# Kernel optimization log

Hardware: AMD Instinct MI355X
Metric: run time of the kernel (lower is better)

Reference implementation:

```python
import jax, jax.numpy as jnp
import numpy as np

KS = 3        # opt.kernel_size
B = 8         # batch
T = 512       # total_length (frames)
CQ = 126      # motion channels
CK = 80       # music channels
H = 128       # hid_c
SLOPE = 0.2   # lrelu slope in ConvBlock
INF = jnp.float32(1e30)


def _conv_block(x, w, b):
    # x: [B, Cin, T]; w: [Cout, Cin, KS]; reflect pad, stride 1, lrelu
    xp = jnp.pad(x, ((0, 0), (0, 0), (1, 1)), mode='reflect')
    y = jax.lax.conv_general_dilated(xp, w, (1,), 'VALID',
                                     dimension_numbers=('NCH', 'OIH', 'NCH'))
    return jax.nn.leaky_relu(y + b[None, :, None], SLOPE)


def _encode(x, params):
    for w, b in params:
        x = _conv_block(x, w, b)
    return x  # [B, H, T]


def _dtw_single(d, L):
    # d: [M, N] cost matrix, L: scalar int valid length. Returns 0/1 path matrix.
    M, N = d.shape
    jcol = jnp.arange(N)
    # row 0: cumulative along j, predecessor is 'left' (choice 1)
    row0 = jnp.cumsum(d[0])
    ch0 = jnp.where(jcol == 0, -1, 1).astype(jnp.int32)

    def row_step(prev_row, d_row):
        p_diag = jnp.concatenate([jnp.full((1,), INF), prev_row[:-1]])

        def inner(left, xs):
            pd, pu, dij, j = xs
            m = jnp.minimum(jnp.minimum(pd, left), pu)
            # tie-break order matches numpy code: diag, then left, then up
            choice = jnp.where(pd == m, 0, jnp.where(left == m, 1, 2)).astype(jnp.int32)
            cost = m + dij
            cost = jnp.where(j == 0, pu + dij, cost)      # first column: from up
            choice = jnp.where(j == 0, 2, choice)
            return cost, (cost, choice)

        _, (crow, chrow) = jax.lax.scan(inner, INF, (p_diag, prev_row, d_row, jcol))
        return crow, chrow

    _, chs = jax.lax.scan(row_step, row0, d[1:])
    choices = jnp.concatenate([ch0[None], chs], axis=0)  # [M, N]

    path01 = jnp.zeros((M, N), jnp.float32).at[L - 1, L - 1].set(1.0)

    def bt_step(carry, _):
        ix, iy, p = carry
        active = (ix > 0) | (iy > 0)
        c = choices[ix, iy]
        nix = jnp.where(c == 0, ix - 1, jnp.where(c == 1, ix, ix - 1))
        niy = jnp.where(c == 0, iy - 1, jnp.where(c == 1, iy - 1, iy))
        nix = jnp.where(active, nix, ix)
        niy = jnp.where(active, niy, iy)
        p = p.at[nix, niy].set(jnp.where(active, 1.0, p[nix, niy]))
        return (nix, niy, p), None

    (_, _, path01), _ = jax.lax.scan(bt_step, (L - 1, L - 1, path01), None,
                                     length=2 * M - 2)
    return path01


def setup_inputs() -> dict:
    key = jax.random.key(0)
    ks = jax.random.split(key, 16)

    def w(k, o, i):
        return jax.random.normal(k, (o, i, KS), jnp.float32) * np.float32(np.sqrt(2.0 / (i * KS)))

    inp = {
        'vec': jax.random.normal(ks[0], (B, CQ, T), jnp.float32),
        'music': jax.random.normal(ks[1], (B, CK, T), jnp.float32),
        'real_length': jax.random.randint(ks[2], (B,), T // 2, T + 1, jnp.int32),
        'qw1': w(ks[3], CQ, CQ), 'qb1': jnp.zeros((CQ,), jnp.float32),
        'qw2': w(ks[4], H, CQ),  'qb2': jnp.zeros((H,), jnp.float32),
        'qw3': w(ks[5], H, H),   'qb3': jnp.zeros((H,), jnp.float32),
        'kw1': w(ks[6], CK, CK), 'kb1': jnp.zeros((CK,), jnp.float32),
        'kw2': w(ks[7], H, CK),  'kb2': jnp.zeros((H,), jnp.float32),
        'kw3': w(ks[8], H, H),   'kb3': jnp.zeros((H,), jnp.float32),
    }
    return inp


def reference(vec, music, real_length, qw1, qb1, qw2, qb2, qw3, qb3,
              kw1, kb1, kw2, kb2, kw3, kb3):
    # conv encoders (ConvBlock x3 each)
    q = _encode(vec, [(qw1, qb1), (qw2, qb2), (qw3, qb3)])    # [B, H, T]
    k = _encode(music, [(kw1, kb1), (kw2, kb2), (kw3, kb3)])  # [B, H, T]
    qf = q.transpose(0, 2, 1)  # [B, N, H] motion latent
    kf = k.transpose(0, 2, 1)  # [B, M, H] music latent
    # Euclidean_dist(music_feat=kf, motion_feat=qf): dist[b, m, n] = ||kf[b,m]-qf[b,n]||
    diff = kf[:, :, None, :] - qf[:, None, :, :]              # [B, M, N, H]
    dist = jnp.sqrt(jnp.sum(diff * diff, axis=-1))            # [B, M, N]
    dist = (dist - dist.min()) / (dist.max() - dist.min())    # global min-max norm
    path01 = jax.vmap(_dtw_single)(dist, real_length)         # [B, M, N]
    return (path01, dist)
```

## Files before the change

kernel.cpp:

```cpp
#include <hip/hip_runtime.h>
#include <hip/hip_bf16.h>

#define T_LEN 512
#define BATCH 8
#define HID 128
#define NSTEP 640

__global__ __launch_bounds__(256) void repack_all_kernel(
    const float* __restrict__ s0, const float* __restrict__ s1,
    const float* __restrict__ s2, const float* __restrict__ s3,
    const float* __restrict__ s4, const float* __restrict__ s5,
    float* __restrict__ out, unsigned* __restrict__ mm)
{
    int i = blockIdx.x * 256 + threadIdx.x;
    if (i == 81412) { mm[0] = 0xFFFFFFFFu; mm[1] = 0u; return; }
    const float* src; int li; float* dst;
    if      (i < 15876) { src = s0; li = i;         dst = out;          }
    else if (i < 32004) { src = s1; li = i - 15876; dst = out + 63504;  }
    else if (i < 48388) { src = s2; li = i - 32004; dst = out + 128016; }
    else if (i < 54788) { src = s3; li = i - 48388; dst = out + 193552; }
    else if (i < 65028) { src = s4; li = i - 54788; dst = out + 219152; }
    else if (i < 81412) { src = s5; li = i - 65028; dst = out + 260112; }
    else return;
    float a = src[li * 3], b = src[li * 3 + 1], c = src[li * 3 + 2];
    *reinterpret_cast<float4*>(dst + li * 4) = make_float4(a, b, c, 0.0f);
}

__global__ __launch_bounds__(512) void conv_dual_kernel(
    const float* __restrict__ xq, const float* __restrict__ wpq,
    const float* __restrict__ bq, float* __restrict__ yq, int CinQ, int CoutQ,
    const float* __restrict__ xk, const float* __restrict__ wpk,
    const float* __restrict__ bk, float* __restrict__ yk, int CinK, int CoutK,
    int ntq)
{
    __shared__ float xs[128 * 66];
    const int b   = blockIdx.z;
    const int t0  = blockIdx.x * 64;
    const int tid = threadIdx.x;
    const int tl  = tid & 63;

    const bool isQ = ((int)blockIdx.y) < ntq;
    const int  yt  = isQ ? blockIdx.y : (blockIdx.y - ntq);
    const float* x  = isQ ? xq  : xk;
    const float* wp = isQ ? wpq : wpk;
    const float* bias = isQ ? bq : bk;
    float* y = isQ ? yq : yk;
    const int Cin  = isQ ? CinQ  : CinK;
    const int Cout = isQ ? CoutQ : CoutK;

    const float* xb = x + (size_t)b * Cin * T_LEN;
    for (int idx = tid; idx < Cin * 66; idx += 512) {
        int ci = idx / 66;
        int tt = idx - ci * 66;
        int g  = t0 + tt - 1;
        g = (g < 0) ? 1 : (g >= T_LEN ? T_LEN - 2 : g);
        xs[idx] = xb[ci * T_LEN + g];
    }
    __syncthreads();

    const int wave = __builtin_amdgcn_readfirstlane(tid >> 6);
    const int co0  = yt * 16 + 2 * wave;
    if (co0 < Cout) {
        const float* __restrict__ wq0 = wp + (size_t)co0 * Cin * 4;
        const float* __restrict__ wq1 = wq0 + Cin * 4;
        float acc0 = 0.0f, acc1 = 0.0f;
#pragma unroll 4
        for (int ci = 0; ci < Cin; ++ci) {
            float xm = xs[ci * 66 + tl];
            float x0 = xs[ci * 66 + tl + 1];
            float xp = xs[ci * 66 + tl + 2];
            const float4 w0 = *reinterpret_cast<const float4*>(wq0 + ci * 4);
            const float4 w1 = *reinterpret_cast<const float4*>(wq1 + ci * 4);
            acc0 = fmaf(w0.x, xm, acc0);
            acc0 = fmaf(w0.y, x0, acc0);
            acc0 = fmaf(w0.z, xp, acc0);
            acc1 = fmaf(w1.x, xm, acc1);
            acc1 = fmaf(w1.y, x0, acc1);
            acc1 = fmaf(w1.z, xp, acc1);
        }
        float v0 = acc0 + bias[co0];
        float v1 = acc1 + bias[co0 + 1];
        v0 = (v0 >= 0.0f) ? v0 : 0.2f * v0;
        v1 = (v1 >= 0.0f) ? v1 : 0.2f * v1;
        y[((size_t)b * Cout + co0) * T_LEN + t0 + tl]     = v0;
        y[((size_t)b * Cout + co0 + 1) * T_LEN + t0 + tl] = v1;
    }
}

__global__ __launch_bounds__(256) void dist_kernel(
    const float* __restrict__ q, const float* __restrict__ k,
    float* __restrict__ dist, unsigned* __restrict__ mm)
{
    __shared__ __align__(16) float ks[HID * 32];
    __shared__ __align__(16) float qs[HID * 32];
    __shared__ float red[8];

    const int b  = blockIdx.z;
    const int m0 = blockIdx.y * 32;
    const int n0 = blockIdx.x * 32;
    const int tid = threadIdx.x;

    const float* qb = q + (size_t)b * HID * T_LEN;
    const float* kb = k + (size_t)b * HID * T_LEN;

    for (int idx = tid; idx < HID * 32; idx += 256) {
        int h = idx >> 5, c = idx & 31;
        ks[idx] = kb[h * T_LEN + m0 + c];
        qs[idx] = qb[h * T_LEN + n0 + c];
    }
    __syncthreads();

    const int nn = tid & 31;
    const int mq = (tid >> 5) * 4;

    float a0 = 0.f, a1 = 0.f, a2 = 0.f, a3 = 0.f;
    for (int h = 0; h < HID; ++h) {
        float qv = qs[h * 32 + nn];
        const float4 kv = *reinterpret_cast<const float4*>(&ks[h * 32 + mq]);
        float d0 = kv.x - qv, d1 = kv.y - qv, d2 = kv.z - qv, d3 = kv.w - qv;
        a0 = fmaf(d0, d0, a0);
        a1 = fmaf(d1, d1, a1);
        a2 = fmaf(d2, d2, a2);
        a3 = fmaf(d3, d3, a3);
    }
    float v0 = sqrtf(a0), v1 = sqrtf(a1), v2 = sqrtf(a2), v3 = sqrtf(a3);

    float* drow = dist + ((size_t)b * T_LEN + m0 + mq) * T_LEN + n0 + nn;
    drow[0 * T_LEN] = v0;
    drow[1 * T_LEN] = v1;
    drow[2 * T_LEN] = v2;
    drow[3 * T_LEN] = v3;

    float mnv = fminf(fminf(v0, v1), fminf(v2, v3));
    float mxv = fmaxf(fmaxf(v0, v1), fmaxf(v2, v3));
#pragma unroll
    for (int off = 32; off >= 1; off >>= 1) {
        mnv = fminf(mnv, __shfl_xor(mnv, off, 64));
        mxv = fmaxf(mxv, __shfl_xor(mxv, off, 64));
    }
    int wid = tid >> 6;
    if ((tid & 63) == 0) { red[wid * 2] = mnv; red[wid * 2 + 1] = mxv; }
    __syncthreads();
    if (tid == 0) {
        float mn = fminf(fminf(red[0], red[2]), fminf(red[4], red[6]));
        float mx = fmaxf(fmaxf(red[1], red[3]), fmaxf(red[5], red[7]));
        atomicMin(&mm[0], __float_as_uint(mn));
        atomicMax(&mm[1], __float_as_uint(mx));
    }
}

__global__ __launch_bounds__(512) void norm_shear_kernel(
    float* __restrict__ dist, float* __restrict__ dsk,
    const unsigned* __restrict__ mm)
{
    __shared__ float tile[64][65];
    const float mn  = __uint_as_float(mm[0]);
    const float rng = __uint_as_float(mm[1]) - mn;
    const int b  = blockIdx.z;
    const int m0 = blockIdx.y * 64;
    const int n0 = blockIdx.x * 64;
    const int tid  = threadIdx.x;
    const int lane = tid & 63;
    const int wv   = tid >> 6;

    float* D = dist + (size_t)b * T_LEN * T_LEN;
#pragma unroll
    for (int r = 0; r < 8; ++r) {
        int lm = wv + r * 8;
        float v = (D[(m0 + lm) * T_LEN + n0 + lane] - mn) / rng;
        D[(m0 + lm) * T_LEN + n0 + lane] = v;
        tile[lm][lane] = v;
    }
    __syncthreads();

    float* dskb = dsk + (size_t)b * NSTEP * T_LEN;
    const int tbase = n0 + (m0 >> 2);
    const int pidx  = (lane & 7) * 64 + (m0 >> 3) + (lane >> 3);
#pragma unroll
    for (int it = 0; it < 10; ++it) {
        int t_local = wv + it * 8;
        int ln = t_local - 2 * (lane >> 3);
        if (t_local <= 78 && ln >= 0 && ln < 64)
            dskb[(size_t)(tbase + t_local) * T_LEN + pidx] = tile[lane][ln];
    }
}

__device__ __forceinline__ void gload_lds16(const float* g, float* l) {
    __builtin_amdgcn_global_load_lds(
        (const __attribute__((address_space(1))) unsigned*)g,
        (__attribute__((address_space(3))) unsigned*)l, 16, 0, 0);
}

#define STAGE(GG, BUFI) do {                                                  \
    const float* gsrc = dskb + (size_t)(GG) * 8 * T_LEN;                      \
    _Pragma("unroll")                                                         \
    for (int rr = 0; rr < 8; ++rr) {                                          \
        gload_lds16(gsrc + rr * T_LEN +   0 + p * 4, &dstage[BUFI][rr][0]);   \
        gload_lds16(gsrc + rr * T_LEN + 256 + p * 4, &dstage[BUFI][rr][256]); \
    }                                                                         \
} while (0)

#define PREF(ARR, BUFI, ROWN) do {                                            \
    _Pragma("unroll")                                                         \
    for (int u = 0; u < 8; ++u) ARR[u] = dstage[BUFI][ROWN][u * 64 + p];      \
} while (0)

#define DTW_STEP_A(T, ARR) do {                                               \
    int j = (T) - 2 * p;                                                      \
    float nut = __shfl_up(L[7], 1, 64);     \
    if ((unsigned)j < 512u) {                                                 \
        int sh = (j & 15) * 2;                                                \
        float cur, oldL, prevrow;                                             \
        unsigned ch;                                                          \
        if (p == 0) {                                                         \
            cur = (j == 0) ? ARR[0] : (L[0] + ARR[0]); ch = 1u;               \
        } else if (j == 0) {                                                  \
            cur = ut + ARR[0]; ch = 2u;                                       \
        } else {                                                              \
            float pd = dt, lf = L[0], pu = ut;                                \
            float m = fminf(fminf(pd, lf), pu);                               \
            ch = (pd == m) ? 0u : ((lf == m) ? 1u : 2u);                      \
            cur = m + ARR[0];                                                 \
        }                                                                     \
        oldL = L[0]; L[0] = cur; prevrow = cur; pk[0] |= ch << sh;            \
        _Pragma("unroll")                                                     \
        for (int u = 1; u < 8; ++u) {                                         \
            if (j == 0) { cur = prevrow + ARR[u]; ch = 2u; }                  \
            else {                                                            \
                float pd = oldL, lf = L[u], pu = prevrow;                     \
                float m = fminf(fminf(pd, lf), pu);                           \
                ch = (pd == m) ? 0u : ((lf == m) ? 1u : 2u);                  \
                cur = m + ARR[u];                                             \
            }                                                                 \
            oldL = L[u]; L[u] = cur; prevrow = cur; pk[u] |= ch << sh;        \
        }                                                                     \
        if ((j & 15) == 15) {                                                 \
            int w4 = (j >> 4) * 4;                                            \
            *reinterpret_cast<uint4*>(&cho[p * 256 + w4]) =                   \
                make_uint4(pk[0], pk[1], pk[2], pk[3]);                       \
            *reinterpret_cast<uint4*>(&cho[p * 256 + 128 + w4]) =             \
                make_uint4(pk[4], pk[5], pk[6], pk[7]);                       \
            pk[0] = pk[1] = pk[2] = pk[3] = 0u;                               \
            pk[4] = pk[5] = pk[6] = pk[7] = 0u;                               \
        }                                                                     \
    }                                                                         \
    dt = ut; ut = nut;                                                        \
} while (0)

__global__ __launch_bounds__(64) void dtw_wave_kernel(
    const float* __restrict__ dsk, const int* __restrict__ rlen,
    float* __restrict__ path)
{
    __shared__ float dstage[2][8][512];
    __shared__ unsigned cho[512 * 32];

    const int b = blockIdx.x;
    const int p = threadIdx.x;
    const float* dskb = dsk + (size_t)b * NSTEP * T_LEN;

    float L[8];
    float ut = 1e30f, dt = 1e30f;
#pragma unroll
    for (int u = 0; u < 8; ++u) L[u] = 1e30f;
    unsigned pk[8] = {0u, 0u, 0u, 0u, 0u, 0u, 0u, 0u};

    STAGE(0, 0);
    STAGE(1, 1);
    asm volatile("s_waitcnt vmcnt(16)" ::: "memory");

    float da[8], db[8], dc[8], dd[8];
    PREF(da, 0, 0);
    PREF(db, 0, 1);

    for (int g = 0; g < 80; ++g) {
        const int cbuf = g & 1, nbuf = cbuf ^ 1;
        const int t0 = g * 8;
        PREF(dc, cbuf, 2); DTW_STEP_A(t0 + 0, da);
        PREF(dd, cbuf, 3); DTW_STEP_A(t0 + 1, db);
        PREF(da, cbuf, 4); DTW_STEP_A(t0 + 2, dc);
        PREF(db, cbuf, 5); DTW_STEP_A(t0 + 3, dd);
        PREF(dc, cbuf, 6); DTW_STEP_A(t0 + 4, da);
        PREF(dd, cbuf, 7); DTW_STEP_A(t0 + 5, db);
        if (g + 2 < 80) {
            STAGE(g + 2, cbuf);
            asm volatile("s_waitcnt vmcnt(16)" ::: "memory");
        } else {
            asm volatile("s_waitcnt vmcnt(0)" ::: "memory");
        }
        PREF(da, nbuf, 0); DTW_STEP_A(t0 + 6, dc);
        PREF(db, nbuf, 1); DTW_STEP_A(t0 + 7, dd);
    }

    __syncthreads();

    if (p == 0) {
        int Lr = rlen[b];
        int ix = Lr - 1, iy = Lr - 1;
        float* po = path + (size_t)b * T_LEN * T_LEN;
        po[ix * T_LEN + iy] = 1.0f;
        while (ix > 0 || iy > 0) {
            uint4 tw = *reinterpret_cast<const uint4*>(
                &cho[((ix >> 2) * 32 + (iy >> 4)) * 4]);
            int tr = ix >> 2, tc = iy >> 4;
            while (true) {
                int sel = ix & 3;
                unsigned wvv = (sel & 2) ? ((sel & 1) ? tw.w : tw.z)
                                         : ((sel & 1) ? tw.y : tw.x);
                int c = (wvv >> ((iy & 15) * 2)) & 3;
                ix -= (c != 1);
                iy -= (c != 2);
                po[ix * T_LEN + iy] = 1.0f;
                if (!(ix > 0 || iy > 0)) break;
                if ((ix >> 2) != tr || (iy >> 4) != tc) break;
            }
        }
    }
}

extern "C" void kernel_launch(void* const* d_in, const int* in_sizes, int n_in,
                              void* d_out, int out_size, void* d_ws, size_t ws_size,
                              hipStream_t stream)
{
    (void)in_sizes; (void)n_in; (void)out_size; (void)ws_size;

    const float* vec   = (const float*)d_in[0];
    const float* music = (const float*)d_in[1];
    const int*   rlen  = (const int*)  d_in[2];
    const float* qw1 = (const float*)d_in[3];  const float* qb1 = (const float*)d_in[4];
    const float* qw2 = (const float*)d_in[5];  const float* qb2 = (const float*)d_in[6];
    const float* qw3 = (const float*)d_in[7];  const float* qb3 = (const float*)d_in[8];
    const float* kw1 = (const float*)d_in[9];  const float* kb1 = (const float*)d_in[10];
    const float* kw2 = (const float*)d_in[11]; const float* kb2 = (const float*)d_in[12];
    const float* kw3 = (const float*)d_in[13]; const float* kb3 = (const float*)d_in[14];

    float* out = (float*)d_out;
    const size_t mat_elems = (size_t)BATCH * T_LEN * T_LEN;
    float* path_out = out;
    float* dist_out = out + mat_elems;

    char* ws = (char*)d_ws;
    const size_t bufB = (size_t)BATCH * HID * T_LEN * sizeof(float);
    float* dsk = (float*)ws;
    float* qA = (float*)(ws + 0 * bufB);
    float* qB = (float*)(ws + 1 * bufB);
    float* kA = (float*)(ws + 2 * bufB);
    float* kB = (float*)(ws + 3 * bufB);
    float* wrep = (float*)(ws + 4 * bufB);
    float* qw1p = wrep;
    float* qw2p = wrep + 63504;
    float* qw3p = wrep + 128016;
    float* kw1p = wrep + 193552;
    float* kw2p = wrep + 219152;
    float* kw3p = wrep + 260112;
    unsigned* mm = (unsigned*)(ws + 10485760);

    hipMemsetAsync(path_out, 0, mat_elems * sizeof(float), stream);

    repack_all_kernel<<<dim3((81413 + 255) / 256), dim3(256), 0, stream>>>(
        qw1, qw2, qw3, kw1, kw2, kw3, wrep, mm);

    dim3 cb(512);
    conv_dual_kernel<<<dim3(8, 13, 8), cb, 0, stream>>>(
        vec, qw1p, qb1, qA, 126, 126, music, kw1p, kb1, kA, 80, 80, 8);
    conv_dual_kernel<<<dim3(8, 16, 8), cb, 0, stream>>>(
        qA, qw2p, qb2, qB, 126, 128, kA, kw2p, kb2, kB, 80, 128, 8);
    conv_dual_kernel<<<dim3(8, 16, 8), cb, 0, stream>>>(
        qB, qw3p, qb3, qA, 128, 128, kB, kw3p, kb3, kA, 128, 128, 8);

    dist_kernel<<<dim3(16, 16, 8), dim3(256), 0, stream>>>(qA, kA, dist_out, mm);

    norm_shear_kernel<<<dim3(8, 8, 8), dim3(512), 0, stream>>>(dist_out, dsk, mm);

    dtw_wave_kernel<<<dim3(BATCH), dim3(64), 0, stream>>>(dsk, rlen, path_out);
}
```

Before: 560.0 us.

## Split DTW wavefront across four waves per batch with LDS boundary handoff

The DTW wavefront kernel now uses four 64-lane waves per batch instead of one. Each wave owns a 128-row band, and each lane holds two rows instead of eight. Waves start in a staggered order and pass their last-row costs to the next wave through an LDS boundary buffer, synchronising with barriers every four 16-step groups. The norm/shear kernel now writes the skewed cost layout per band to match. This shortens each lane's serial dependency chain per step, at the cost of pipeline fill from the staggered starts and extra barriers.

```diff
diff --git a/kernel.cpp b/kernel.cpp
--- a/kernel.cpp
+++ b/kernel.cpp
@@ -5,6 +5,9 @@
 #define BATCH 8
 #define HID 128
 #define NSTEP 640
+#define NGRP 40
+#define SSOFF 3
+#define TOTSS 19
 
 __global__ __launch_bounds__(256) void repack_all_kernel(
     const float* __restrict__ s0, const float* __restrict__ s1,
@@ -153,7 +156,7 @@
     float* __restrict__ dist, float* __restrict__ dsk,
     const unsigned* __restrict__ mm)
 {
-    __shared__ float tile[64][65];
+    __shared__ float tile[64][66];
     const float mn  = __uint_as_float(mm[0]);
     const float rng = __uint_as_float(mm[1]) - mn;
     const int b  = blockIdx.z;
@@ -173,15 +176,16 @@
     }
     __syncthreads();
 
-    float* dskb = dsk + (size_t)b * NSTEP * T_LEN;
-    const int tbase = n0 + (m0 >> 2);
-    const int pidx  = (lane & 7) * 64 + (m0 >> 3) + (lane >> 3);
+    const int w  = m0 >> 7;
+    const int c0 = m0 & 127;
+    float* dskw = dsk + ((size_t)(b * 4 + w) * NSTEP) * 128;
+    const int tb = n0 + c0;
 #pragma unroll
-    for (int it = 0; it < 10; ++it) {
+    for (int it = 0; it < 16; ++it) {
         int t_local = wv + it * 8;
-        int ln = t_local - 2 * (lane >> 3);
-        if (t_local <= 78 && ln >= 0 && ln < 64)
-            dskb[(size_t)(tbase + t_local) * T_LEN + pidx] = tile[lane][ln];
+        int ln = t_local - 2 * (lane >> 1);
+        if (t_local <= 125 && ln >= 0 && ln < 64)
+            dskw[(size_t)(tb + t_local) * 128 + c0 + lane] = tile[lane][ln];
     }
 }
 
@@ -191,109 +195,139 @@
         (__attribute__((address_space(3))) unsigned*)l, 16, 0, 0);
 }
 
-#define STAGE(GG, BUFI) do {                                                  \
-    const float* gsrc = dskb + (size_t)(GG) * 8 * T_LEN;                      \
+#define STAGE(GG) do {                                                        \
+    const float* gsrc = dskw + (size_t)(GG) * (16 * 128);                     \
+    float* ldst = &dstage[w][(GG) & 1][0][0];                                 \
     _Pragma("unroll")                                                         \
-    for (int rr = 0; rr < 8; ++rr) {                                          \
-        gload_lds16(gsrc + rr * T_LEN +   0 + p * 4, &dstage[BUFI][rr][0]);   \
-        gload_lds16(gsrc + rr * T_LEN + 256 + p * 4, &dstage[BUFI][rr][256]); \
-    }                                                                         \
+    for (int rr = 0; rr < 8; ++rr)                                            \
+        gload_lds16(gsrc + rr * 256 + p * 4, ldst + rr * 256);                \
 } while (0)
 
-#define PREF(ARR, BUFI, ROWN) do {                                            \
-    _Pragma("unroll")                                                         \
-    for (int u = 0; u < 8; ++u) ARR[u] = dstage[BUFI][ROWN][u * 64 + p];      \
+#define PREF2(N0, N1, BUF, S) do {                                            \
+    float2 _t = *reinterpret_cast<const float2*>(&dstage[w][BUF][S][2 * p]);  \
+    N0 = _t.x; N1 = _t.y;                                                     \
 } while (0)
 
-#define DTW_STEP_A(T, ARR) do {                                               \
-    int j = (T) - 2 * p;                                                      \
-    float nut = __shfl_up(L[7], 1, 64);     \
+#define STEP(T, F0, F1) do {                                                  \
+    const int T_ = (T);                                                       \
+    int j = T_ - 2 * p;                                                       \
+    float nut = __shfl_up(L1, 1, 64);                                         \
+    float nbv = browp[(T_ + 1 < 512) ? (T_ + 1) : 511];                       \
+    if (hasb && p == 0) nut = nbv;                                            \
     if ((unsigned)j < 512u) {                                                 \
         int sh = (j & 15) * 2;                                                \
-        float cur, oldL, prevrow;                                             \
-        unsigned ch;                                                          \
-        if (p == 0) {                                                         \
-            cur = (j == 0) ? ARR[0] : (L[0] + ARR[0]); ch = 1u;               \
+        float cur0; unsigned ch0;                                             \
+        if (isw0 && p == 0) {                                                 \
+            cur0 = (j == 0) ? F0 : (L0 + F0); ch0 = 1u;                       \
         } else if (j == 0) {                                                  \
-            cur = ut + ARR[0]; ch = 2u;                                       \
+            cur0 = ut + F0; ch0 = 2u;                                         \
         } else {                                                              \
-            float pd = dt, lf = L[0], pu = ut;                                \
-            float m = fminf(fminf(pd, lf), pu);                               \
-            ch = (pd == m) ? 0u : ((lf == m) ? 1u : 2u);                      \
-            cur = m + ARR[0];                                                 \
+            float m = fminf(fminf(dt, L0), ut);                               \
+            ch0 = (dt == m) ? 0u : ((L0 == m) ? 1u : 2u);                     \
+            cur0 = m + F0;                                                    \
         }                                                                     \
-        oldL = L[0]; L[0] = cur; prevrow = cur; pk[0] |= ch << sh;            \
-        _Pragma("unroll")                                                     \
-        for (int u = 1; u < 8; ++u) {                                         \
-            if (j == 0) { cur = prevrow + ARR[u]; ch = 2u; }                  \
-            else {                                                            \
-                float pd = oldL, lf = L[u], pu = prevrow;                     \
-                float m = fminf(fminf(pd, lf), pu);                           \
-                ch = (pd == m) ? 0u : ((lf == m) ? 1u : 2u);                  \
-                cur = m + ARR[u];                                             \
-            }                                                                 \
-            oldL = L[u]; L[u] = cur; prevrow = cur; pk[u] |= ch << sh;        \
+        float cur1; unsigned ch1;                                             \
+        if (j == 0) { cur1 = cur0 + F1; ch1 = 2u; }                           \
+        else {                                                                \
+            float m1 = fminf(fminf(L0, L1), cur0);                            \
+            ch1 = (L0 == m1) ? 0u : ((L1 == m1) ? 1u : 2u);                   \
+            cur1 = m1 + F1;                                                   \
         }                                                                     \
+        L0 = cur0; L1 = cur1;                                                 \
+        pk0 |= ch0 << sh; pk1 |= ch1 << sh;                                   \
         if ((j & 15) == 15) {                                                 \
-            int w4 = (j >> 4) * 4;                                            \
-            *reinterpret_cast<uint4*>(&cho[p * 256 + w4]) =                   \
-                make_uint4(pk[0], pk[1], pk[2], pk[3]);                       \
-            *reinterpret_cast<uint4*>(&cho[p * 256 + 128 + w4]) =             \
-                make_uint4(pk[4], pk[5], pk[6], pk[7]);                       \
-            pk[0] = pk[1] = pk[2] = pk[3] = 0u;                               \
-            pk[4] = pk[5] = pk[6] = pk[7] = 0u;                               \
+            unsigned long long pw = (unsigned long long)pk0 |                 \
+                                    ((unsigned long long)pk1 << 32);          \
+            *reinterpret_cast<unsigned long long*>(                           \
+                &cho[chobase + (j >> 4) * 4]) = pw;                           \
+            pk0 = 0u; pk1 = 0u;                                               \
         }                                                                     \
     }                                                                         \
     dt = ut; ut = nut;                                                        \
+    if (wlt3 && p == 63) {                                                    \
+        int j63 = T_ - 126;                                                   \
+        if ((unsigned)j63 < 512u) broww[j63] = L1;                            \
+    }                                                                         \
 } while (0)
 
-__global__ __launch_bounds__(64) void dtw_wave_kernel(
+#define GROUP16(TB, BUF, NBUF, DOSTAGE, GS) do {                              \
+    PREF2(C0, C1, BUF, 2);  STEP((TB) + 0, A0, A1);                           \
+    PREF2(D0, D1, BUF, 3);  STEP((TB) + 1, B0, B1);                           \
+    PREF2(A0, A1, BUF, 4);  STEP((TB) + 2, C0, C1);                           \
+    PREF2(B0, B1, BUF, 5);  STEP((TB) + 3, D0, D1);                           \
+    PREF2(C0, C1, BUF, 6);  STEP((TB) + 4, A0, A1);                           \
+    PREF2(D0, D1, BUF, 7);  STEP((TB) + 5, B0, B1);                           \
+    PREF2(A0, A1, BUF, 8);  STEP((TB) + 6, C0, C1);                           \
+    PREF2(B0, B1, BUF, 9);  STEP((TB) + 7, D0, D1);                           \
+    PREF2(C0, C1, BUF, 10); STEP((TB) + 8, A0, A1);                           \
+    PREF2(D0, D1, BUF, 11); STEP((TB) + 9, B0, B1);                           \
+    PREF2(A0, A1, BUF, 12); STEP((TB) + 10, C0, C1);                          \
+    PREF2(B0, B1, BUF, 13); STEP((TB) + 11, D0, D1);                          \
+    PREF2(C0, C1, BUF, 14); STEP((TB) + 12, A0, A1);                          \
+    PREF2(D0, D1, BUF, 15); STEP((TB) + 13, B0, B1);                          \
+    if (DOSTAGE) {                                                            \
+        STAGE(GS);                                                            \
+        asm volatile("s_waitcnt vmcnt(8)" ::: "memory");                      \
+    } else {                                                                  \
+        asm volatile("s_waitcnt vmcnt(0)" ::: "memory");                      \
+    }                                                                         \
+    PREF2(A0, A1, NBUF, 0); STEP((TB) + 14, C0, C1);                          \
+    PREF2(B0, B1, NBUF, 1); STEP((TB) + 15, D0, D1);                          \
+} while (0)
+
+__global__ __launch_bounds__(256) void dtw_wave_kernel(
     const float* __restrict__ dsk, const int* __restrict__ rlen,
     float* __restrict__ path)
 {
-    __shared__ float dstage[2][8][512];
+    __shared__ float dstage[4][2][16][128];
     __shared__ unsigned cho[512 * 32];
-
-    const int b = blockIdx.x;
-    const int p = threadIdx.x;
-    const float* dskb = dsk + (size_t)b * NSTEP * T_LEN;
-
-    float L[8];
-    float ut = 1e30f, dt = 1e30f;
-#pragma unroll
-    for (int u = 0; u < 8; ++u) L[u] = 1e30f;
-    unsigned pk[8] = {0u, 0u, 0u, 0u, 0u, 0u, 0u, 0u};
-
-    STAGE(0, 0);
-    STAGE(1, 1);
-    asm volatile("s_waitcnt vmcnt(16)" ::: "memory");
-
-    float da[8], db[8], dc[8], dd[8];
-    PREF(da, 0, 0);
-    PREF(db, 0, 1);
-
-    for (int g = 0; g < 80; ++g) {
-        const int cbuf = g & 1, nbuf = cbuf ^ 1;
-        const int t0 = g * 8;
-        PREF(dc, cbuf, 2); DTW_STEP_A(t0 + 0, da);
-        PREF(dd, cbuf, 3); DTW_STEP_A(t0 + 1, db);
-        PREF(da, cbuf, 4); DTW_STEP_A(t0 + 2, dc);
-        PREF(db, cbuf, 5); DTW_STEP_A(t0 + 3, dd);
-        PREF(dc, cbuf, 6); DTW_STEP_A(t0 + 4, da);
-        PREF(dd, cbuf, 7); DTW_STEP_A(t0 + 5, db);
-        if (g + 2 < 80) {
-            STAGE(g + 2, cbuf);
-            asm volatile("s_waitcnt vmcnt(16)" ::: "memory");
-        } else {
-            asm volatile("s_waitcnt vmcnt(0)" ::: "memory");
+    __shared__ float brow[3][512];
+
+    const int b   = blockIdx.x;
+    const int tid = threadIdx.x;
+    const int w   = __builtin_amdgcn_readfirstlane(tid >> 6);
+    const int p   = tid & 63;
+
+    const float* dskw = dsk + ((size_t)(b * 4 + w) * NSTEP) * 128;
+    const bool isw0 = (w == 0);
+    const bool hasb = (w > 0);
+    const bool wlt3 = (w < 3);
+    const float* browp = &brow[hasb ? (w - 1) : 0][0];
+    float* broww = &brow[wlt3 ? w : 0][0];
+    const int chobase = (32 * w + (p >> 1)) * 128 + 2 * (p & 1);
+
+    float L0 = 1e30f, L1 = 1e30f, ut = 1e30f, dt = 1e30f;
+    unsigned pk0 = 0u, pk1 = 0u;
+    float A0, A1, B0, B1, C0, C1, D0, D1;
+    A0 = A1 = B0 = B1 = C0 = C1 = D0 = D1 = 0.0f;
+
+    STAGE(0);
+    STAGE(1);
+
+    int G = 0;
+    for (int g = 0; g < TOTSS; ++g) {
+        if (g >= SSOFF * w && G < NGRP) {
+            if (g == SSOFF * w) {
+                if (hasb) ut = browp[0];
+                asm volatile("s_waitcnt vmcnt(8)" ::: "memory");
+                PREF2(A0, A1, 0, 0);
+                PREF2(B0, B1, 0, 1);
+            }
+            for (int q = 0; q < 4; ++q) {
+                const int tb   = G * 16;
+                const int buf  = G & 1;
+                const int nbuf = buf ^ 1;
+                const bool dostage = (G + 2 < NGRP);
+                GROUP16(tb, buf, nbuf, dostage, G + 2);
+                ++G;
+            }
         }
-        PREF(da, nbuf, 0); DTW_STEP_A(t0 + 6, dc);
-        PREF(db, nbuf, 1); DTW_STEP_A(t0 + 7, dd);
-    }
-
-    __syncthreads();
-
-    if (p == 0) {
+        asm volatile("s_waitcnt lgkmcnt(0)" ::: "memory");
+        __builtin_amdgcn_s_barrier();
+        __builtin_amdgcn_sched_barrier(0);
+    }
+
+    if (tid == 0) {
         int Lr = rlen[b];
         int ix = Lr - 1, iy = Lr - 1;
         float* po = path + (size_t)b * T_LEN * T_LEN;
@@ -371,5 +405,5 @@
 
     norm_shear_kernel<<<dim3(8, 8, 8), dim3(512), 0, stream>>>(dist_out, dsk, mm);
 
-    dtw_wave_kernel<<<dim3(BATCH), dim3(64), 0, stream>>>(dsk, rlen, path_out);
-}
+    dtw_wave_kernel<<<dim3(BATCH), dim3(256), 0, stream>>>(dsk, rlen, path_out);
+}
```

Result: faster. 531.2 us (-5.1%).
